# Kernel tuning notes

Measured on AMD Instinct MI355X. Metric: run time of the kernel, lower is better.

The kernel has to match this reference:

```python
import jax, jax.numpy as jnp
import numpy as np

N_ATOMS, N_BONDS, MAX_NB = 100_000, 200_000, 6
ATOM_FDIM, BOND_FDIM = 133, 147
HIDDEN, DEPTH = 256, 3
N_MOLS, MOL_FEAT = 4096, 200
FFNN_HID, ENC_HID = 512, 256


def setup_inputs() -> dict:
    key = jax.random.key(0)
    ks = jax.random.split(key, 12)
    f_atoms = jax.random.normal(ks[0], (N_ATOMS, ATOM_FDIM), jnp.float32)
    f_bonds = jax.random.normal(ks[1], (N_BONDS, BOND_FDIM), jnp.float32)
    a2b = jax.random.randint(ks[2], (N_ATOMS, MAX_NB), 0, N_BONDS, jnp.int32)
    b2a = jax.random.randint(ks[3], (N_BONDS,), 0, N_ATOMS, jnp.int32)
    # reverse bond of directed bond i is its pair partner (i XOR 1)
    b2revb = (jnp.arange(N_BONDS, dtype=jnp.int32) ^ 1)
    atom2mol = jnp.sort(jax.random.randint(ks[4], (N_ATOMS,), 0, N_MOLS, jnp.int32))
    mol_features = jax.random.normal(ks[5], (N_MOLS, MOL_FEAT), jnp.float32)
    # weights stored as [in, out]
    W_i = jax.random.normal(ks[6], (BOND_FDIM, HIDDEN), jnp.float32) / np.sqrt(BOND_FDIM)
    W_h = jax.random.normal(ks[7], (HIDDEN, HIDDEN), jnp.float32) / np.sqrt(HIDDEN)
    W_o_w = jax.random.normal(ks[8], (ATOM_FDIM + HIDDEN, HIDDEN), jnp.float32) / np.sqrt(ATOM_FDIM + HIDDEN)
    W_o_b = jnp.zeros((HIDDEN,), jnp.float32)
    W1 = jax.random.normal(ks[9], (HIDDEN + MOL_FEAT, FFNN_HID), jnp.float32) / np.sqrt(HIDDEN + MOL_FEAT)
    b1 = jnp.zeros((FFNN_HID,), jnp.float32)
    W2 = jax.random.normal(ks[10], (FFNN_HID, ENC_HID), jnp.float32) / np.sqrt(FFNN_HID)
    b2 = jnp.zeros((ENC_HID,), jnp.float32)
    return dict(f_atoms=f_atoms, f_bonds=f_bonds, a2b=a2b, b2a=b2a, b2revb=b2revb,
                atom2mol=atom2mol, mol_features=mol_features,
                W_i=W_i, W_h=W_h, W_o_w=W_o_w, W_o_b=W_o_b,
                W1=W1, b1=b1, W2=W2, b2=b2)


def reference(f_atoms, f_bonds, a2b, b2a, b2revb, atom2mol, mol_features,
              W_i, W_h, W_o_w, W_o_b, W1, b1, W2, b2):
    n_mols = mol_features.shape[0]
    inputs = f_bonds @ W_i                      # [B, H]
    message = jax.nn.relu(inputs)
    for _ in range(DEPTH - 1):
        nei = message[a2b]                      # [A, MAX_NB, H] gather
        a_message = nei.sum(axis=1)             # [A, H]
        message = jax.nn.relu(inputs + (a_message[b2a] - message[b2revb]) @ W_h)
    nei = message[a2b]
    a_message = nei.sum(axis=1)                 # [A, H]
    a_input = jnp.concatenate([f_atoms, a_message], axis=1)
    atom_hiddens = jax.nn.relu(a_input @ W_o_w + W_o_b)  # [A, H]
    # per-molecule mean; empty molecules -> zero vector (cached_zero_vector)
    sums = jax.ops.segment_sum(atom_hiddens, atom2mol, num_segments=n_mols)
    counts = jax.ops.segment_sum(jnp.ones((atom_hiddens.shape[0],), atom_hiddens.dtype),
                                 atom2mol, num_segments=n_mols)
    mol_vecs = sums / jnp.maximum(counts, 1.0)[:, None]  # [n_mols, H]
    x = jnp.concatenate([mol_vecs, mol_features], axis=1)
    h = jax.nn.relu(x @ W1 + b1)
    out = jax.nn.relu(h @ W2 + b2)
    return out
```

## Files before the change

### kernel.cpp

```cpp
#include <hip/hip_runtime.h>
#include <hip/hip_bf16.h>


typedef __hip_bfloat16 bf16;
typedef __attribute__((ext_vector_type(8))) short short8;
typedef __attribute__((ext_vector_type(4))) short short4v;
typedef __attribute__((ext_vector_type(4))) float f32x4;
typedef __attribute__((ext_vector_type(4), aligned(4))) float f32x4u;

__device__ __forceinline__ float b2f(bf16 x) { return __bfloat162float(x); }
__device__ __forceinline__ bf16  f2b(float x) { return __float2bfloat16(x); }
__device__ __forceinline__ float bs2f(short s) {
    unsigned int u = ((unsigned int)(unsigned short)s) << 16;
    float f; __builtin_memcpy(&f, &u, 4); return f;
}
__device__ __forceinline__ short f2bs(float f) {
    bf16 b = __float2bfloat16(f);
    short s; __builtin_memcpy(&s, &b, 2); return s;
}

#define GRID 256
#define TR 32

template <int KP, int MODE, bool RELU, int ADDC, bool HASBIAS, bool OUTF32>
__global__ __launch_bounds__(512, 1) void gemm_wres(
    int M, int ntiles, int Ktrue,
    const float* __restrict__ Af,
    const bf16* __restrict__ Ab1, const bf16* __restrict__ Ab2,
    const int* __restrict__ g1, const int* __restrict__ g2,
    const bf16* __restrict__ Wt,
    const float* __restrict__ bias,
    const bf16* __restrict__ addB, const float* __restrict__ addF,
    bf16* __restrict__ outB, float* __restrict__ outF)
{
    constexpr int NK  = KP / 32;
    constexpr int NU  = KP / 8;
    constexpr int KP2 = KP * 2;
    __shared__ bf16 Wl[256 * KP];
    __shared__ bf16 At[TR * KP];

    const int t = threadIdx.x;
    int tile = blockIdx.x;
    if (tile >= ntiles) return;

    {
        int n = t >> 1, half = t & 1;
        const short8* src = (const short8*)(Wt + (size_t)n * KP) + half * (NU / 2);
        char* dst = (char*)Wl + (size_t)n * KP2;
        #pragma unroll
        for (int i = 0; i < NU / 2; i++) {
            int g = half * (NU / 2) + i;
            *(short8*)(dst + ((g ^ (n & 7)) << 4)) = src[i];
        }
    }
    __syncthreads();

    const int wave = t >> 6, lane = t & 63;
    const int mrow = lane & 15, kq = lane >> 4;
    const int r = t >> 4, j = t & 15;

    float biasReg[2] = {0.f, 0.f};
    if (HASBIAS) {
        #pragma unroll
        for (int tn = 0; tn < 2; tn++)
            biasReg[tn] = bias[wave * 32 + tn * 16 + mrow];
    }

    short8 pA[2], pB[2];
    f32x4  pF[3];
    short8 pC[2];

    auto prefA = [&](int tl) {
        int row = tl * TR + r;
        if (MODE == 1) {
            int r1 = g1[row], r2 = g2[row];
            const char* s1 = (const char*)(Ab1 + ((size_t)r1 << 8));
            const char* s2 = (const char*)(Ab2 + ((size_t)r2 << 8));
            #pragma unroll
            for (int u = 0; u < 2; u++) {
                pA[u] = *(const short8*)(s1 + ((j + 16 * u) << 4));
                pB[u] = *(const short8*)(s2 + ((j + 16 * u) << 4));
            }
        } else if (MODE == 2) {
            const char* s1 = (const char*)(Ab1 + ((size_t)row << 8));
            #pragma unroll
            for (int u = 0; u < 2; u++)
                pA[u] = *(const short8*)(s1 + ((j + 16 * u) << 4));
        } else {
            const float* src = Af + (size_t)row * Ktrue;
            #pragma unroll
            for (int v = 0; v < 3; v++) {
                int c = j + 16 * v;
                f32x4 val = {0.f, 0.f, 0.f, 0.f};
                if (c * 4 < Ktrue) {
                    if (row == M - 1 && c * 4 + 4 > Ktrue) {
                        #pragma unroll
                        for (int e = 0; e < 4; e++)
                            if (c * 4 + e < Ktrue) val[e] = src[c * 4 + e];
                    } else {
                        val = *(const f32x4u*)(src + c * 4);
                    }
                }
                pF[v] = val;
            }
        }
    };
    auto prefAdd = [&](int tl) {
        int row = tl * TR + r;
        const char* s = (const char*)(addB + ((size_t)row << 8));
        #pragma unroll
        for (int u = 0; u < 2; u++)
            pC[u] = *(const short8*)(s + ((j + 16 * u) << 4));
    };
    auto convWrite = [&]() {
        char* dst = (char*)At + (size_t)r * KP2;
        if (MODE == 1) {
            #pragma unroll
            for (int u = 0; u < 2; u++) {
                short8 a = pA[u], b = pB[u], o;
                #pragma unroll
                for (int e = 0; e < 8; e++)
                    o[e] = f2bs(bs2f(a[e]) - fmaxf(bs2f(b[e]), 0.f));
                int g = j + 16 * u;
                *(short8*)(dst + ((g ^ (r & 7)) << 4)) = o;
            }
        } else if (MODE == 2) {
            #pragma unroll
            for (int u = 0; u < 2; u++) {
                int g = j + 16 * u;
                *(short8*)(dst + ((g ^ (r & 7)) << 4)) = pA[u];
            }
        } else {
            #pragma unroll
            for (int v = 0; v < 3; v++) {
                int c = j + 16 * v;
                f32x4 x = pF[v];
                short4v o;
                #pragma unroll
                for (int e = 0; e < 4; e++) o[e] = f2bs(x[e]);
                int unit = c >> 1, sub = (c & 1) << 3;
                *(short4v*)(dst + ((unit ^ (r & 7)) << 4) + sub) = o;
            }
        }
    };

    prefA(tile);
    for (;;) {
        convWrite();
        __syncthreads();
        const int nxt = tile + GRID;
        const bool more = nxt < ntiles;
        if (ADDC == 1) prefAdd(tile);
        if (more) prefA(nxt);

        f32x4 acc[2][2] = {};
        #pragma unroll
        for (int ks = 0; ks < NK; ks++) {
            short8 afr[2], bfr[2];
            #pragma unroll
            for (int tm = 0; tm < 2; tm++) {
                int arow = tm * 16 + mrow;
                afr[tm] = *(const short8*)((char*)At + (size_t)arow * KP2 +
                            (((ks * 4 + kq) ^ (arow & 7)) << 4));
            }
            #pragma unroll
            for (int tn = 0; tn < 2; tn++) {
                int n = wave * 32 + tn * 16 + mrow;
                bfr[tn] = *(const short8*)((char*)Wl + (size_t)n * KP2 +
                            (((ks * 4 + kq) ^ (n & 7)) << 4));
            }
            #pragma unroll
            for (int tm = 0; tm < 2; tm++)
                #pragma unroll
                for (int tn = 0; tn < 2; tn++)
                    acc[tm][tn] = __builtin_amdgcn_mfma_f32_16x16x32_bf16(
                        afr[tm], bfr[tn], acc[tm][tn], 0, 0, 0);
        }
        __syncthreads();

        if (ADDC == 1) {
            char* dst = (char*)At + (size_t)r * KP2;
            #pragma unroll
            for (int u = 0; u < 2; u++) {
                int g = j + 16 * u;
                *(short8*)(dst + ((g ^ (r & 7)) << 4)) = pC[u];
            }
            __syncthreads();
        }

        const int bm = tile * TR;
        #pragma unroll
        for (int tm = 0; tm < 2; tm++) {
            #pragma unroll
            for (int rr = 0; rr < 4; rr++) {
                int lrow = tm * 16 + kq * 4 + rr;
                size_t rb = (size_t)(bm + lrow) << 8;
                #pragma unroll
                for (int tn = 0; tn < 2; tn++) {
                    int col = wave * 32 + tn * 16 + mrow;
                    float v = acc[tm][tn][rr];
                    if (HASBIAS) v += biasReg[tn];
                    if (ADDC == 1) {
                        int u = col >> 3;
                        short s = *(const short*)((char*)At + (size_t)lrow * KP2 +
                                   ((u ^ (lrow & 7)) << 4) + ((col & 7) << 1));
                        v += bs2f(s);
                    } else if (ADDC == 2) {
                        v += addF[rb + col];
                    }
                    if (RELU) v = fmaxf(v, 0.f);
                    if (OUTF32) outF[rb + col] = v;
                    else        outB[rb + col] = f2b(v);
                }
            }
        }
        if (!more) break;
        if (ADDC == 1) __syncthreads();
        tile = nxt;
    }
}

__global__ __launch_bounds__(256) void convert_wt(
    const float* __restrict__ W, bf16* __restrict__ Wt, int K, int Koff, int Kp)
{
    int i = blockIdx.x * 256 + threadIdx.x;
    if (i >= 256 * Kp) return;
    int n = i / Kp, k = i - n * Kp;
    Wt[i] = (k < K) ? f2b(W[(size_t)(k + Koff) * 256 + n]) : f2b(0.f);
}

__global__ __launch_bounds__(256) void gather_sum8(
    const bf16* __restrict__ msg, const int* __restrict__ a2b,
    bf16* __restrict__ amsg, int A)
{
    int idx = blockIdx.x * 256 + threadIdx.x;
    if (idx >= A * 32) return;
    int a  = idx >> 5;
    int c8 = (idx & 31) * 8;
    const int* nb = a2b + (size_t)a * 6;
    float s[8] = {};
    #pragma unroll
    for (int k = 0; k < 6; k++) {
        const short8 v = *(const short8*)(msg + ((size_t)nb[k] << 8) + c8);
        #pragma unroll
        for (int e = 0; e < 8; e++) s[e] += fmaxf(bs2f(v[e]), 0.f);
    }
    short8 o;
    #pragma unroll
    for (int e = 0; e < 8; e++) o[e] = f2bs(s[e]);
    *(short8*)(amsg + ((size_t)a << 8) + c8) = o;
}

#define K3 1536

__global__ __launch_bounds__(256) void conv_w3(
    const float* __restrict__ W, bf16* __restrict__ Wp, int K, int N)
{
    int idx = blockIdx.x * 256 + threadIdx.x;
    if (idx >= N * 512) return;
    int n = idx >> 9, k = idx & 511;
    float w = (k < K) ? W[(size_t)k * N + n] : 0.f;
    bf16 hi = f2b(w);
    bf16 lo = f2b(w - b2f(hi));
    size_t base = (size_t)n * K3;
    Wp[base + k] = hi;
    Wp[base + 512 + k] = hi;
    Wp[base + 1024 + k] = lo;
}

__global__ __launch_bounds__(256) void conv_feat(
    const float* __restrict__ mf, bf16* __restrict__ A1p)
{
    int idx = blockIdx.x * 256 + threadIdx.x;
    int m = idx >> 8, j = idx & 255;
    float v = (j < 200) ? mf[(size_t)m * 200 + j] : 0.f;
    bf16 hi = f2b(v);
    bf16 lo = f2b(v - b2f(hi));
    size_t base = (size_t)m * K3 + 256;
    A1p[base + j] = hi;
    A1p[base + 512 + j] = lo;
    A1p[base + 1024 + j] = hi;
}

__global__ __launch_bounds__(256) void segment_mean3(
    const bf16* __restrict__ ah, const int* __restrict__ atom2mol,
    int A, bf16* __restrict__ A1p)
{
    int m = blockIdx.x;
    int h = threadIdx.x;
    int lo_ = 0, hi_ = A;
    while (lo_ < hi_) { int mid = (lo_ + hi_) >> 1; if (atom2mol[mid] < m) lo_ = mid + 1; else hi_ = mid; }
    int start = lo_;
    hi_ = A;
    while (lo_ < hi_) { int mid = (lo_ + hi_) >> 1; if (atom2mol[mid] <= m) lo_ = mid + 1; else hi_ = mid; }
    int end = lo_;
    float s = 0.f;
    for (int a = start; a < end; a++) s += b2f(ah[(size_t)a * 256 + h]);
    float mean = s / fmaxf((float)(end - start), 1.f);
    bf16 hi = f2b(mean);
    bf16 lo = f2b(mean - b2f(hi));
    size_t base = (size_t)m * K3;
    A1p[base + h] = hi;
    A1p[base + 512 + h] = lo;
    A1p[base + 1024 + h] = hi;
}

template <bool OUT3>
__global__ __launch_bounds__(256, 2) void gemm3(
    int N,
    const bf16* __restrict__ Ap, const bf16* __restrict__ Wp,
    const float* __restrict__ bias,
    bf16* __restrict__ out3, float* __restrict__ outF)
{
    __shared__ bf16 As[2][64 * 64];
    __shared__ bf16 Bs[2][64 * 64];

    const int t = threadIdx.x;
    const int bm = blockIdx.x * 64, bn = blockIdx.y * 64;
    const int row = t >> 2, q = t & 3;
    const bf16* srcA = Ap + (size_t)(bm + row) * K3 + q * 16;
    const bf16* srcB = Wp + (size_t)(bn + row) * K3 + q * 16;

    short8 ra[2], rb[2];
    auto LOADT = [&](int t0) {
        #pragma unroll
        for (int u = 0; u < 2; u++) {
            ra[u] = *(const short8*)(srcA + t0 * 64 + u * 8);
            rb[u] = *(const short8*)(srcB + t0 * 64 + u * 8);
        }
    };
    auto WRITET = [&](int buf) {
        char* da = (char*)&As[buf][0] + row * 128;
        char* db = (char*)&Bs[buf][0] + row * 128;
        #pragma unroll
        for (int u = 0; u < 2; u++) {
            int g = q * 2 + u;
            *(short8*)(da + ((g ^ (row & 7)) << 4)) = ra[u];
            *(short8*)(db + ((g ^ (row & 7)) << 4)) = rb[u];
        }
    };

    const int wave = t >> 6, lane = t & 63;
    const int mrow = lane & 15, kq = lane >> 4;
    const int wm = (wave >> 1) * 32, wn = (wave & 1) * 32;

    f32x4 acc[2][2] = {};
    LOADT(0);
    WRITET(0);

    for (int t0 = 0; t0 < K3 / 64; t0++) {
        const int cur = t0 & 1;
        __syncthreads();
        if (t0 + 1 < K3 / 64) LOADT(t0 + 1);
        #pragma unroll
        for (int ks = 0; ks < 2; ks++) {
            short8 af[2], bfr[2];
            #pragma unroll
            for (int i = 0; i < 2; i++) {
                int ar = wm + i * 16 + mrow;
                af[i] = *(const short8*)((char*)&As[cur][0] + ar * 128 +
                          (((ks * 4 + kq) ^ (ar & 7)) << 4));
            }
            #pragma unroll
            for (int jx = 0; jx < 2; jx++) {
                int br = wn + jx * 16 + mrow;
                bfr[jx] = *(const short8*)((char*)&Bs[cur][0] + br * 128 +
                          (((ks * 4 + kq) ^ (br & 7)) << 4));
            }
            #pragma unroll
            for (int i = 0; i < 2; i++)
                #pragma unroll
                for (int jx = 0; jx < 2; jx++)
                    acc[i][jx] = __builtin_amdgcn_mfma_f32_16x16x32_bf16(
                        af[i], bfr[jx], acc[i][jx], 0, 0, 0);
        }
        if (t0 + 1 < K3 / 64) WRITET(cur ^ 1);
    }

    #pragma unroll
    for (int i = 0; i < 2; i++) {
        #pragma unroll
        for (int r = 0; r < 4; r++) {
            int grow = bm + wm + i * 16 + kq * 4 + r;
            #pragma unroll
            for (int jx = 0; jx < 2; jx++) {
                int gcol = bn + wn + jx * 16 + mrow;
                float v = acc[i][jx][r] + bias[gcol];
                v = fmaxf(v, 0.f);
                if (OUT3) {
                    bf16 hi = f2b(v);
                    bf16 lo = f2b(v - b2f(hi));
                    size_t base = (size_t)grow * K3;
                    out3[base + gcol] = hi;
                    out3[base + 512 + gcol] = lo;
                    out3[base + 1024 + gcol] = hi;
                } else {
                    outF[(size_t)grow * N + gcol] = v;
                }
            }
        }
    }
}

extern "C" void kernel_launch(void* const* d_in, const int* in_sizes, int n_in,
                              void* d_out, int out_size, void* d_ws, size_t ws_size,
                              hipStream_t stream)
{
    const float* f_atoms  = (const float*)d_in[0];
    const float* f_bonds  = (const float*)d_in[1];
    const int*   a2b      = (const int*)d_in[2];
    const int*   b2a      = (const int*)d_in[3];
    const int*   b2revb   = (const int*)d_in[4];
    const int*   atom2mol = (const int*)d_in[5];
    const float* mol_feat = (const float*)d_in[6];
    const float* W_i      = (const float*)d_in[7];
    const float* W_h      = (const float*)d_in[8];
    const float* W_o_w    = (const float*)d_in[9];
    const float* W_o_b    = (const float*)d_in[10];
    const float* W1       = (const float*)d_in[11];
    const float* b1       = (const float*)d_in[12];
    const float* W2       = (const float*)d_in[13];
    const float* b2       = (const float*)d_in[14];

    const int A  = 100000, B = 200000, H = 256;
    const int AF = 133, BF = 147;
    const int NM = 4096, FH = 512, EH = 256;
    const int KpS = 192;
    const int KpH = 256;

    char* ws = (char*)d_ws;
    bf16* buf0 = (bf16*)ws;  ws += (size_t)B * H * sizeof(bf16);
    bf16* buf1 = (bf16*)ws;  ws += (size_t)B * H * sizeof(bf16);
    bf16* amsg = (bf16*)ws;  ws += (size_t)A * H * sizeof(bf16);
    bf16* WtI  = (bf16*)ws;  ws += (size_t)256 * KpS * sizeof(bf16);
    bf16* WtH  = (bf16*)ws;  ws += (size_t)256 * KpH * sizeof(bf16);
    bf16* WtO1 = (bf16*)ws;  ws += (size_t)256 * KpS * sizeof(bf16);
    bf16* WtO2 = (bf16*)ws;  ws += (size_t)256 * KpH * sizeof(bf16);
    bf16* W1p  = (bf16*)ws;  ws += (size_t)FH * K3 * sizeof(bf16);
    bf16* W2p  = (bf16*)ws;  ws += (size_t)EH * K3 * sizeof(bf16);
    float* fbuf = (float*)buf1;
    bf16* A1p = buf0;
    bf16* A2p = buf0 + (size_t)NM * K3;

    dim3 blk(256), blkG(512);
    const int ntB = B / TR;
    const int ntA = A / TR;
    const int gsG = (A * 32 + 255) / 256;

    convert_wt<<<dim3((256 * KpS + 255) / 256), blk, 0, stream>>>(W_i,   WtI,  BF,  0,  KpS);
    convert_wt<<<dim3((256 * KpH + 255) / 256), blk, 0, stream>>>(W_h,   WtH,  H,   0,  KpH);
    convert_wt<<<dim3((256 * KpS + 255) / 256), blk, 0, stream>>>(W_o_w, WtO1, AF,  0,  KpS);
    convert_wt<<<dim3((256 * KpH + 255) / 256), blk, 0, stream>>>(W_o_w, WtO2, H,   AF, KpH);
    conv_w3<<<dim3((FH * 512 + 255) / 256), blk, 0, stream>>>(W1, W1p, H + 200, FH);
    conv_w3<<<dim3((EH * 512 + 255) / 256), blk, 0, stream>>>(W2, W2p, FH, EH);

    gemm_wres<192, 0, false, 0, false, false><<<dim3(GRID), blkG, 0, stream>>>(
        B, ntB, BF, f_bonds, nullptr, nullptr, nullptr, nullptr,
        WtI, nullptr, nullptr, nullptr, buf0, nullptr);

    gather_sum8<<<dim3(gsG), blk, 0, stream>>>(buf0, a2b, amsg, A);
    gemm_wres<256, 1, true, 1, false, false><<<dim3(GRID), blkG, 0, stream>>>(
        B, ntB, H, nullptr, amsg, buf0, b2a, b2revb,
        WtH, nullptr, buf0, nullptr, buf1, nullptr);

    gather_sum8<<<dim3(gsG), blk, 0, stream>>>(buf1, a2b, amsg, A);
    gemm_wres<256, 1, true, 1, false, false><<<dim3(GRID), blkG, 0, stream>>>(
        B, ntB, H, nullptr, amsg, buf1, b2a, b2revb,
        WtH, nullptr, buf0, nullptr, buf0, nullptr);

    gather_sum8<<<dim3(gsG), blk, 0, stream>>>(buf0, a2b, amsg, A);

    conv_feat<<<dim3(NM), blk, 0, stream>>>(mol_feat, A1p);

    gemm_wres<192, 0, false, 0, false, true><<<dim3(GRID), blkG, 0, stream>>>(
        A, ntA, AF, f_atoms, nullptr, nullptr, nullptr, nullptr,
        WtO1, nullptr, nullptr, nullptr, nullptr, fbuf);

    gemm_wres<256, 2, true, 2, true, false><<<dim3(GRID), blkG, 0, stream>>>(
        A, ntA, H, nullptr, amsg, nullptr, nullptr, nullptr,
        WtO2, W_o_b, nullptr, fbuf, amsg, nullptr);

    segment_mean3<<<dim3(NM), blk, 0, stream>>>(amsg, atom2mol, A, A1p);

    gemm3<true><<<dim3(NM / 64, FH / 64), blk, 0, stream>>>(
        FH, A1p, W1p, b1, A2p, nullptr);

    gemm3<false><<<dim3(NM / 64, EH / 64), blk, 0, stream>>>(
        EH, A2p, W2p, b2, nullptr, (float*)d_out);
}
```

Measured before the change: 696.7 us.

## Hold GEMM weights in registers, double-buffer A tiles, raise occupancy

The weight matrix now stays in per-wave registers (wreg) instead of a 256xKP LDS copy, which frees LDS. The A tile is double-buffered so one barrier per tile is enough. The bf16 residual add now reads straight from global memory rather than being staged through LDS. With the smaller LDS footprint, the grid doubles to 512 persistent blocks and launch bounds allow 4 blocks per CU, raising occupancy; the costs are higher register pressure (possible spills at KP=256) and uncoalesced 2-byte residual loads.

```diff
diff --git a/kernel.cpp b/kernel.cpp
--- a/kernel.cpp
+++ b/kernel.cpp
@@ -19,11 +19,11 @@
     short s; __builtin_memcpy(&s, &b, 2); return s;
 }
 
-#define GRID 256
+#define GRID 512
 #define TR 32
 
 template <int KP, int MODE, bool RELU, int ADDC, bool HASBIAS, bool OUTF32>
-__global__ __launch_bounds__(512, 1) void gemm_wres(
+__global__ __launch_bounds__(512, 4) void gemm_wres(
     int M, int ntiles, int Ktrue,
     const float* __restrict__ Af,
     const bf16* __restrict__ Ab1, const bf16* __restrict__ Ab2,
@@ -34,31 +34,25 @@
     bf16* __restrict__ outB, float* __restrict__ outF)
 {
     constexpr int NK  = KP / 32;
-    constexpr int NU  = KP / 8;
     constexpr int KP2 = KP * 2;
-    __shared__ bf16 Wl[256 * KP];
-    __shared__ bf16 At[TR * KP];
+    __shared__ bf16 At[2][TR * KP];
 
     const int t = threadIdx.x;
     int tile = blockIdx.x;
     if (tile >= ntiles) return;
 
-    {
-        int n = t >> 1, half = t & 1;
-        const short8* src = (const short8*)(Wt + (size_t)n * KP) + half * (NU / 2);
-        char* dst = (char*)Wl + (size_t)n * KP2;
-        #pragma unroll
-        for (int i = 0; i < NU / 2; i++) {
-            int g = half * (NU / 2) + i;
-            *(short8*)(dst + ((g ^ (n & 7)) << 4)) = src[i];
-        }
-    }
-    __syncthreads();
-
     const int wave = t >> 6, lane = t & 63;
     const int mrow = lane & 15, kq = lane >> 4;
     const int r = t >> 4, j = t & 15;
 
+    short8 wreg[2][NK];
+    #pragma unroll
+    for (int tn = 0; tn < 2; tn++) {
+        const bf16* wp = Wt + (size_t)(wave * 32 + tn * 16 + mrow) * KP + kq * 8;
+        #pragma unroll
+        for (int ks = 0; ks < NK; ks++)
+            wreg[tn][ks] = *(const short8*)(wp + ks * 32);
+    }
     float biasReg[2] = {0.f, 0.f};
     if (HASBIAS) {
         #pragma unroll
@@ -68,7 +62,6 @@
 
     short8 pA[2], pB[2];
     f32x4  pF[3];
-    short8 pC[2];
 
     auto prefA = [&](int tl) {
         int row = tl * TR + r;
@@ -105,15 +98,8 @@
             }
         }
     };
-    auto prefAdd = [&](int tl) {
-        int row = tl * TR + r;
-        const char* s = (const char*)(addB + ((size_t)row << 8));
-        #pragma unroll
-        for (int u = 0; u < 2; u++)
-            pC[u] = *(const short8*)(s + ((j + 16 * u) << 4));
-    };
-    auto convWrite = [&]() {
-        char* dst = (char*)At + (size_t)r * KP2;
+    auto convWrite = [&](int buf) {
+        char* dst = (char*)&At[buf][0] + (size_t)r * KP2;
         if (MODE == 1) {
             #pragma unroll
             for (int u = 0; u < 2; u++) {
@@ -145,47 +131,30 @@
     };
 
     prefA(tile);
+    int cur = 0;
     for (;;) {
-        convWrite();
+        convWrite(cur);
         __syncthreads();
         const int nxt = tile + GRID;
         const bool more = nxt < ntiles;
-        if (ADDC == 1) prefAdd(tile);
         if (more) prefA(nxt);
 
         f32x4 acc[2][2] = {};
         #pragma unroll
         for (int ks = 0; ks < NK; ks++) {
-            short8 afr[2], bfr[2];
+            short8 afr[2];
             #pragma unroll
             for (int tm = 0; tm < 2; tm++) {
-                int arow = tm * 16 + mrow;
-                afr[tm] = *(const short8*)((char*)At + (size_t)arow * KP2 +
-                            (((ks * 4 + kq) ^ (arow & 7)) << 4));
-            }
-            #pragma unroll
-            for (int tn = 0; tn < 2; tn++) {
-                int n = wave * 32 + tn * 16 + mrow;
-                bfr[tn] = *(const short8*)((char*)Wl + (size_t)n * KP2 +
-                            (((ks * 4 + kq) ^ (n & 7)) << 4));
+                int ar = tm * 16 + mrow;
+                afr[tm] = *(const short8*)((char*)&At[cur][0] + (size_t)ar * KP2 +
+                            (((ks * 4 + kq) ^ (ar & 7)) << 4));
             }
             #pragma unroll
             for (int tm = 0; tm < 2; tm++)
                 #pragma unroll
                 for (int tn = 0; tn < 2; tn++)
                     acc[tm][tn] = __builtin_amdgcn_mfma_f32_16x16x32_bf16(
-                        afr[tm], bfr[tn], acc[tm][tn], 0, 0, 0);
-        }
-        __syncthreads();
-
-        if (ADDC == 1) {
-            char* dst = (char*)At + (size_t)r * KP2;
-            #pragma unroll
-            for (int u = 0; u < 2; u++) {
-                int g = j + 16 * u;
-                *(short8*)(dst + ((g ^ (r & 7)) << 4)) = pC[u];
-            }
-            __syncthreads();
+                        afr[tm], wreg[tn][ks], acc[tm][tn], 0, 0, 0);
         }
 
         const int bm = tile * TR;
@@ -193,21 +162,14 @@
         for (int tm = 0; tm < 2; tm++) {
             #pragma unroll
             for (int rr = 0; rr < 4; rr++) {
-                int lrow = tm * 16 + kq * 4 + rr;
-                size_t rb = (size_t)(bm + lrow) << 8;
+                size_t rb = (size_t)(bm + tm * 16 + kq * 4 + rr) << 8;
                 #pragma unroll
                 for (int tn = 0; tn < 2; tn++) {
                     int col = wave * 32 + tn * 16 + mrow;
                     float v = acc[tm][tn][rr];
                     if (HASBIAS) v += biasReg[tn];
-                    if (ADDC == 1) {
-                        int u = col >> 3;
-                        short s = *(const short*)((char*)At + (size_t)lrow * KP2 +
-                                   ((u ^ (lrow & 7)) << 4) + ((col & 7) << 1));
-                        v += bs2f(s);
-                    } else if (ADDC == 2) {
-                        v += addF[rb + col];
-                    }
+                    if (ADDC == 1)      v += b2f(addB[rb + col]);
+                    else if (ADDC == 2) v += addF[rb + col];
                     if (RELU) v = fmaxf(v, 0.f);
                     if (OUTF32) outF[rb + col] = v;
                     else        outB[rb + col] = f2b(v);
@@ -215,8 +177,8 @@
             }
         }
         if (!more) break;
-        if (ADDC == 1) __syncthreads();
         tile = nxt;
+        cur ^= 1;
     }
 }
 
```

Measured after the change: 726.8 us. +4.3%, slower.
